# Performance work log

Measured on AMD Instinct MI355X. Metric: run time of the kernel, lower is better.

The kernel has to match this reference:

```python
import jax, jax.numpy as jnp
import numpy as np

B, T, D, E, K = 4, 2048, 2048, 8, 2
H = 4 * D  # expert hidden dim


def setup_inputs() -> dict:
    key = jax.random.key(0)
    ks = jax.random.split(key, 12)
    s = 0.02  # weight init scale
    return {
        "x": jax.random.normal(ks[0], (B, T, D), dtype=jnp.float32),
        "eps": jax.random.normal(ks[1], (B, T, E), dtype=jnp.float32),
        "Wr": jax.random.normal(ks[2], (D, E), dtype=jnp.float32) * s,
        "br": jnp.zeros((E,), dtype=jnp.float32),
        "Wn": jax.random.normal(ks[3], (D, E), dtype=jnp.float32) * s,
        "bn": jnp.zeros((E,), dtype=jnp.float32),
        "W1": jax.random.normal(ks[4], (E, D, H), dtype=jnp.float32) * s,
        "b1": jnp.zeros((E, H), dtype=jnp.float32),
        "W2": jax.random.normal(ks[5], (E, H, D), dtype=jnp.float32) * s,
        "b2": jnp.zeros((E, D), dtype=jnp.float32),
    }


def _moe(x, eps, Wr, br, Wn, bn, W1, b1, W2, b2):
    # --- noisy top-k router ---
    logits = x @ Wr + br                                   # [B,T,E]
    noise_logits = x @ Wn + bn                             # [B,T,E]
    noisy = logits + eps * jax.nn.softplus(noise_logits)   # [B,T,E]
    _, top_idx = jax.lax.top_k(noisy, K)                   # [B,T,K]
    sel = jax.nn.one_hot(top_idx, E, dtype=noisy.dtype).sum(-2)  # [B,T,E] 0/1
    neg_inf = jnp.asarray(-jnp.inf, dtype=noisy.dtype)
    sparse_logits = jnp.where(sel > 0, noisy, neg_inf)
    gates = jax.nn.softmax(sparse_logits, axis=-1)         # zeros off the top-k
    # --- expert MLPs, combined with gates (gate==0 exactly when unrouted,
    #     matching the torch masked gather/scatter; dropout in eval mode) ---
    out = jnp.zeros_like(x)
    for i in range(E):  # fixed small expert count
        h = jax.nn.relu(x @ W1[i] + b1[i])                 # [B,T,H]
        y = h @ W2[i] + b2[i]                              # [B,T,D]
        out = out + y * gates[..., i:i + 1]
    return out


def reference(x, eps, Wr, br, Wn, bn, W1, b1, W2, b2):
    return _moe(x, eps, Wr, br, Wn, bn, W1, b1, W2, b2)
```

## Files before the change

### kernel.cpp

```cpp
#include <hip/hip_runtime.h>

#define BT_TOK 8192
#define DDIM   2048
#define EEXP   8
#define HDIM   8192
#define MAXT1  72
#define MAXT2  144

typedef __bf16 bf16x8 __attribute__((ext_vector_type(8)));
typedef float  f32x4  __attribute__((ext_vector_type(4)));

__device__ inline ushort f2bf(float f) {
  unsigned u = __float_as_uint(f);
  u += 0x7FFFu + ((u >> 16) & 1u);
  return (ushort)(u >> 16);
}

__device__ __forceinline__ void gl16(const ushort* g, ushort* l) {
  __builtin_amdgcn_global_load_lds(
      (const __attribute__((address_space(1))) void*)g,
      (__attribute__((address_space(3))) void*)l, 16, 0, 0);
}

__global__ __launch_bounds__(256) void k_router(
    const float* __restrict__ x, const float* __restrict__ eps,
    const float* __restrict__ Wr, const float* __restrict__ br,
    const float* __restrict__ Wn, const float* __restrict__ bn,
    int* __restrict__ cnt, int* __restrict__ tk_e, int* __restrict__ tk_p,
    float* __restrict__ tk_g)
{
  const int lane = threadIdx.x & 63;
  const int t = blockIdx.x * 4 + (threadIdx.x >> 6);
  const float* xr = x + (size_t)t * DDIM;
  float aL[8] = {0,0,0,0,0,0,0,0};
  float aN[8] = {0,0,0,0,0,0,0,0};
  for (int i = lane; i < DDIM; i += 64) {
    float xv = xr[i];
    const float4* wr4 = (const float4*)(Wr + (size_t)i * EEXP);
    const float4* wn4 = (const float4*)(Wn + (size_t)i * EEXP);
    float4 r0 = wr4[0], r1 = wr4[1];
    float4 n0 = wn4[0], n1 = wn4[1];
    aL[0] += xv * r0.x; aL[1] += xv * r0.y; aL[2] += xv * r0.z; aL[3] += xv * r0.w;
    aL[4] += xv * r1.x; aL[5] += xv * r1.y; aL[6] += xv * r1.z; aL[7] += xv * r1.w;
    aN[0] += xv * n0.x; aN[1] += xv * n0.y; aN[2] += xv * n0.z; aN[3] += xv * n0.w;
    aN[4] += xv * n1.x; aN[5] += xv * n1.y; aN[6] += xv * n1.z; aN[7] += xv * n1.w;
  }
  #pragma unroll
  for (int e = 0; e < 8; ++e) {
    float v = aL[e];
    #pragma unroll
    for (int s = 32; s; s >>= 1) v += __shfl_xor(v, s);
    aL[e] = v;
    float w = aN[e];
    #pragma unroll
    for (int s = 32; s; s >>= 1) w += __shfl_xor(w, s);
    aN[e] = w;
  }
  float nz[8];
  #pragma unroll
  for (int e = 0; e < 8; ++e) {
    float l = aL[e] + br[e];
    float z = aN[e] + bn[e];
    float sp = fmaxf(z, 0.f) + log1pf(expf(-fabsf(z)));
    nz[e] = l + eps[(size_t)t * EEXP + e] * sp;
  }
  int e1 = 0; float v1 = nz[0];
  #pragma unroll
  for (int e = 1; e < 8; ++e) if (nz[e] > v1) { v1 = nz[e]; e1 = e; }
  int e2 = (e1 == 0) ? 1 : 0; float v2 = nz[e2];
  #pragma unroll
  for (int e = 0; e < 8; ++e) if (e != e1 && nz[e] > v2) { v2 = nz[e]; e2 = e; }
  float ex = expf(v2 - v1);
  float g1 = 1.f / (1.f + ex);
  float g2 = ex / (1.f + ex);
  if (lane == 0) {
    int p1 = atomicAdd(&cnt[e1], 1);
    int p2 = atomicAdd(&cnt[e2], 1);
    tk_e[t * 2 + 0] = e1; tk_p[t * 2 + 0] = p1; tk_g[t * 2 + 0] = g1;
    tk_e[t * 2 + 1] = e2; tk_p[t * 2 + 1] = p2; tk_g[t * 2 + 1] = g2;
  }
}

__global__ void k_off(const int* __restrict__ cnt, int* __restrict__ off,
                      int* __restrict__ tm1, int* __restrict__ tm2,
                      int* __restrict__ ntl) {
  if (threadIdx.x == 0 && blockIdx.x == 0) {
    int a = 0, n1 = 0, n2 = 0;
    for (int e = 0; e < EEXP; ++e) {
      off[e] = a;
      int mt = (cnt[e] + 255) >> 8;
      for (int m = 0; m < mt; ++m) {
        tm1[n1++] = (e << 8) | (m << 1);
        tm2[n2++] = (e << 8) | (m << 1);
        tm2[n2++] = (e << 8) | (m << 1) | 1;
      }
      a += cnt[e];
    }
    off[EEXP] = a;
    ntl[0] = n1; ntl[1] = n2;
  }
}

__global__ __launch_bounds__(256) void k_gather(
    const float* __restrict__ x, const int* __restrict__ off,
    const int* __restrict__ tk_e, const int* __restrict__ tk_p,
    const float* __restrict__ tk_g,
    int* __restrict__ slt, float* __restrict__ gate, ushort* __restrict__ xg)
{
  const int b = blockIdx.x;
  const int t = b >> 1;
  const int e = tk_e[b];
  const int slot = off[e] + tk_p[b];
  if (threadIdx.x == 0) { slt[b] = slot; gate[slot] = tk_g[b]; }
  const float4* src = (const float4*)(x + (size_t)t * DDIM);
  ushort* dst = xg + (size_t)slot * DDIM;
  const int i = threadIdx.x;
  float4 a = src[i * 2 + 0];
  float4 c = src[i * 2 + 1];
  union { ushort u[8]; uint4 q; } pk;
  pk.u[0] = f2bf(a.x); pk.u[1] = f2bf(a.y); pk.u[2] = f2bf(a.z); pk.u[3] = f2bf(a.w);
  pk.u[4] = f2bf(c.x); pk.u[5] = f2bf(c.y); pk.u[6] = f2bf(c.z); pk.u[7] = f2bf(c.w);
  *(uint4*)(dst + (size_t)i * 8) = pk.q;
}

__global__ __launch_bounds__(256) void k_transpose(
    const float* __restrict__ W, ushort* __restrict__ Wt, int R, int C)
{
  const int e = blockIdx.z;
  const float* We = W + (size_t)e * R * C;
  ushort* Wte = Wt + (size_t)e * R * C;
  const int r0 = blockIdx.y * 64, c0 = blockIdx.x * 64;
  __shared__ float tile[64][65];
  const int tx = threadIdx.x & 15, ty = threadIdx.x >> 4;
  #pragma unroll
  for (int p = 0; p < 4; ++p) {
    float4 v = *(const float4*)(We + (size_t)(r0 + p * 16 + ty) * C + c0 + tx * 4);
    tile[p * 16 + ty][tx * 4 + 0] = v.x;
    tile[p * 16 + ty][tx * 4 + 1] = v.y;
    tile[p * 16 + ty][tx * 4 + 2] = v.z;
    tile[p * 16 + ty][tx * 4 + 3] = v.w;
  }
  __syncthreads();
  const int c = threadIdx.x >> 2, rb = (threadIdx.x & 3) * 16;
  union { ushort u[16]; uint4 q[2]; } pk;
  #pragma unroll
  for (int j = 0; j < 16; ++j) pk.u[j] = f2bf(tile[rb + j][c]);
  uint4* dst = (uint4*)(Wte + (size_t)(c0 + c) * R + r0 + rb);
  dst[0] = pk.q[0];
  dst[1] = pk.q[1];
}


#define MFMA_(a, b, c) __builtin_amdgcn_mfma_f32_16x16x32_bf16(a, b, c, 0, 0, 0)
#define DSR(D, A) asm volatile("ds_read_b128 %0, %1" : "=v"(D) : "v"(A))
#define MQ(MB, NB, AV, BV) do {                                                  \
    _Pragma("unroll")                                                            \
    for (int i_ = 0; i_ < 4; ++i_) {                                             \
      acc[(MB)+i_][(NB)]   = MFMA_(AV[2*i_],   BV[0], acc[(MB)+i_][(NB)]);       \
      acc[(MB)+i_][(NB)+1] = MFMA_(AV[2*i_],   BV[2], acc[(MB)+i_][(NB)+1]);     \
    }                                                                            \
    _Pragma("unroll")                                                            \
    for (int i_ = 0; i_ < 4; ++i_) {                                             \
      acc[(MB)+i_][(NB)]   = MFMA_(AV[2*i_+1], BV[1], acc[(MB)+i_][(NB)]);       \
      acc[(MB)+i_][(NB)+1] = MFMA_(AV[2*i_+1], BV[3], acc[(MB)+i_][(NB)+1]);     \
    }                                                                            \
  } while (0)

template<int KD, int KSPLIT, int EPI, int NDIM>
__global__ __launch_bounds__(512, 2) void k_gemm(
    const ushort* __restrict__ A, const ushort* __restrict__ B,
    const float* __restrict__ bias, const int* __restrict__ off,
    const int* __restrict__ tileMap, const int* __restrict__ nT,
    const float* __restrict__ gate,
    ushort* __restrict__ Hout, float* __restrict__ Y)
{
  constexpr int KS = KD / KSPLIT;
  constexpr int NKT = KS / 64;
  constexpr int NTN = NDIM / 256;
  __shared__ ushort lds[65536];
  const int TM = nT[0];
  const int T = TM * NTN;

  const int bid = blockIdx.x;
  const int xcd = bid & 7, sl = bid >> 3;
  const int qq = T >> 3, rr = T & 7;
  const int base = xcd * qq + (xcd < rr ? xcd : rr);
  const int csz = qq + (xcd < rr ? 1 : 0);

  const int tid = threadIdx.x;
  const int lane = tid & 63, wid = tid >> 6;
  const int wm = wid >> 2, wn = wid & 3;
  const int fr = lane & 15, q2 = lane >> 4;
  const unsigned lbase =
      (unsigned)(size_t)(__attribute__((address_space(3))) ushort*)lds;
  const int swz = (q2 ^ (fr & 7)) * 16;
  const int aoff0 = (int)lbase + wm * 16384 + fr * 128 + swz;
  const int boff0 = (int)lbase + 32768 + wn * 8192 + fr * 128 + swz;
  const int trow = tid >> 3;
  const int kx = ((tid & 7) ^ (trow & 7)) * 8;
  const int dstA = tid * 8;

#define STG(SRC, DUS) gl16((SRC), &lds[DUS])

  for (int it = sl; it < csz; it += 32) {
    const int f = base + it;
    const int ni = (int)((unsigned)f / (unsigned)TM);
    const int pk = tileMap[f - ni * TM];
    const int e = pk >> 8, mi = (pk >> 1) & 127, kh = pk & 1;
    const int o = off[e], n_e = off[e + 1] - o;
    const int m0 = mi * 256;
    const int k0 = kh * KS;

    const ushort* Bex = B + (size_t)e * NDIM * KD + (size_t)ni * 256 * KD + k0 + kx;
    const ushort* aS[4]; const ushort* bS[4];
    #pragma unroll
    for (int j = 0; j < 4; ++j) {
      int ar = m0 + j * 64 + trow;
      if (ar > n_e - 1) ar = n_e - 1;
      aS[j] = A + (size_t)(o + ar) * KD + k0 + kx;
      bS[j] = Bex + (size_t)(j * 64 + trow) * KD;
    }

    f32x4 acc[8][4];
    #pragma unroll
    for (int m = 0; m < 8; ++m)
      #pragma unroll
      for (int n = 0; n < 4; ++n) acc[m][n] = (f32x4){0.f, 0.f, 0.f, 0.f};

    bf16x8 avL[8], avH[8], bvL[4], bvH[4];

    STG(aS[0], 0 + dstA);        STG(aS[2], 8192 + dstA);
    STG(aS[1], 4096 + dstA);     STG(aS[3], 12288 + dstA);
    STG(bS[0], 16384 + dstA);    STG(bS[1], 20480 + dstA);
    STG(bS[2], 24576 + dstA);    STG(bS[3], 28672 + dstA);
    STG(aS[0] + 64, 32768 + 0 + dstA);     STG(aS[2] + 64, 32768 + 8192 + dstA);
    STG(aS[1] + 64, 32768 + 4096 + dstA);  STG(aS[3] + 64, 32768 + 12288 + dstA);
    STG(bS[0] + 64, 32768 + 16384 + dstA); STG(bS[1] + 64, 32768 + 20480 + dstA);
    STG(bS[2] + 64, 32768 + 24576 + dstA); STG(bS[3] + 64, 32768 + 28672 + dstA);
    asm volatile("s_waitcnt vmcnt(8)");
    __builtin_amdgcn_s_barrier();
    __builtin_amdgcn_sched_barrier(0);
    {
      const int aA = aoff0, bA = boff0;
      DSR(avL[0], aA);        DSR(avL[1], aA ^ 64);
      DSR(avL[2], aA + 2048); DSR(avL[3], (aA + 2048) ^ 64);
      DSR(avL[4], aA + 4096); DSR(avL[5], (aA + 4096) ^ 64);
      DSR(avL[6], aA + 6144); DSR(avL[7], (aA + 6144) ^ 64);
      DSR(bvL[0], bA);        DSR(bvL[1], bA ^ 64);
      DSR(bvL[2], bA + 2048); DSR(bvL[3], (bA + 2048) ^ 64);
    }

    #pragma unroll 1
    for (int t = 0; t < NKT; ++t) {
      const int bb = (t & 1) << 16;
      const int aA = aoff0 + bb;
      const int bA = boff0 + bb;
      const int nbB = ((t + 1) & 1) << 16;
      const int aN = aoff0 + nbB;
      const int bN = boff0 + nbB;
      const int cbu = (t & 1) * 32768;
      const size_t ko = (size_t)(t + 2) * 64;
      const bool pf = (t + 2 < NKT);
      const bool rd1 = (t + 1 < NKT);

      DSR(avH[0], aA + 8192);         DSR(avH[1], (aA + 8192) ^ 64);
      DSR(avH[2], aA + 10240);        DSR(avH[3], (aA + 10240) ^ 64);
      DSR(avH[4], aA + 12288);        DSR(avH[5], (aA + 12288) ^ 64);
      DSR(avH[6], aA + 14336);        DSR(avH[7], (aA + 14336) ^ 64);
      __builtin_amdgcn_s_barrier();
      asm volatile("s_waitcnt lgkmcnt(8)");
      __builtin_amdgcn_sched_barrier(0);
      if (pf) { STG(aS[0] + ko, cbu + 0 + dstA); STG(aS[2] + ko, cbu + 8192 + dstA); }
      __builtin_amdgcn_s_setprio(1);
      MQ(0, 0, avL, bvL);
      __builtin_amdgcn_s_setprio(0);

      DSR(bvH[0], bA + 4096);  DSR(bvH[1], (bA + 4096) ^ 64);
      DSR(bvH[2], bA + 6144);  DSR(bvH[3], (bA + 6144) ^ 64);
      __builtin_amdgcn_s_barrier();
      asm volatile("s_waitcnt lgkmcnt(4)");
      __builtin_amdgcn_sched_barrier(0);
      if (pf) { STG(aS[1] + ko, cbu + 4096 + dstA); STG(aS[3] + ko, cbu + 12288 + dstA); }
      __builtin_amdgcn_s_setprio(1);
      MQ(4, 0, avH, bvL);
      __builtin_amdgcn_s_setprio(0);

      if (pf) asm volatile("s_waitcnt vmcnt(4)");
      else    asm volatile("s_waitcnt vmcnt(0)");
      __builtin_amdgcn_s_barrier();
      asm volatile("s_waitcnt lgkmcnt(0)");
      __builtin_amdgcn_sched_barrier(0);
      if (pf) {
        STG(bS[0] + ko, cbu + 16384 + dstA); STG(bS[1] + ko, cbu + 20480 + dstA);
        STG(bS[2] + ko, cbu + 24576 + dstA); STG(bS[3] + ko, cbu + 28672 + dstA);
      }
      __builtin_amdgcn_s_setprio(1);
      MQ(0, 2, avL, bvH);
      __builtin_amdgcn_s_setprio(0);
      if (rd1) {
        DSR(avL[0], aN);        DSR(avL[1], aN ^ 64);
        DSR(avL[2], aN + 2048); DSR(avL[3], (aN + 2048) ^ 64);
        DSR(avL[4], aN + 4096); DSR(avL[5], (aN + 4096) ^ 64);
        DSR(avL[6], aN + 6144); DSR(avL[7], (aN + 6144) ^ 64);
      }

      __builtin_amdgcn_s_barrier();
      __builtin_amdgcn_sched_barrier(0);
      if (rd1) {
        DSR(bvL[0], bN);        DSR(bvL[1], bN ^ 64);
        DSR(bvL[2], bN + 2048); DSR(bvL[3], (bN + 2048) ^ 64);
      }
      __builtin_amdgcn_s_setprio(1);
      MQ(4, 2, avH, bvH);
      __builtin_amdgcn_s_setprio(0);
    }

    asm volatile("s_waitcnt vmcnt(0)");
    const int colBase = ni * 256 + wn * 64 + fr;
    const int rBase = m0 + wm * 128 + q2 * 4;
    float bb4[4];
    #pragma unroll
    for (int n = 0; n < 4; ++n) {
      if constexpr (EPI == 0)
        bb4[n] = bias[(size_t)e * NDIM + colBase + n * 16];
      else
        bb4[n] = (kh == 0) ? bias[(size_t)e * NDIM + colBase + n * 16] : 0.f;
    }

    if constexpr (EPI == 0) {
      #pragma unroll
      for (int m = 0; m < 8; ++m) {
        #pragma unroll
        for (int jj = 0; jj < 4; ++jj) {
          int r = rBase + m * 16 + jj;
          if (r < n_e) {
            ushort* hp = Hout + (size_t)(o + r) * NDIM + colBase;
            #pragma unroll
            for (int n = 0; n < 4; ++n)
              hp[n * 16] = f2bf(fmaxf(acc[m][n][jj] + bb4[n], 0.f));
          }
        }
      }
    } else {
      float* yk = Y + ((size_t)kh << 25);
      #pragma unroll
      for (int m = 0; m < 8; ++m) {
        #pragma unroll
        for (int jj = 0; jj < 4; ++jj) {
          int r = rBase + m * 16 + jj;
          if (r < n_e) {
            float g = gate[o + r];
            float* yp = yk + (size_t)(o + r) * NDIM + colBase;
            #pragma unroll
            for (int n = 0; n < 4; ++n)
              yp[n * 16] = g * (acc[m][n][jj] + bb4[n]);
          }
        }
      }
    }
  }
#undef STG
}

__global__ __launch_bounds__(256) void k_combine(
    const float* __restrict__ Y, const int* __restrict__ slt,
    float* __restrict__ out)
{
  const int t = blockIdx.x;
  const int c = threadIdx.x * 8;
  const int sA = slt[t * 2], sB = slt[t * 2 + 1];
  const float4* pA0 = (const float4*)(Y + (size_t)sA * DDIM + c);
  const float4* pB0 = (const float4*)(Y + (size_t)sB * DDIM + c);
  const float4* pA1 = (const float4*)(Y + ((size_t)1 << 25) + (size_t)sA * DDIM + c);
  const float4* pB1 = (const float4*)(Y + ((size_t)1 << 25) + (size_t)sB * DDIM + c);
  float4* op = (float4*)(out + (size_t)t * DDIM + c);
  #pragma unroll
  for (int j = 0; j < 2; ++j) {
    float4 a = pA0[j], b = pA1[j], cc = pB0[j], d = pB1[j];
    float4 r;
    r.x = a.x + b.x + cc.x + d.x;
    r.y = a.y + b.y + cc.y + d.y;
    r.z = a.z + b.z + cc.z + d.z;
    r.w = a.w + b.w + cc.w + d.w;
    op[j] = r;
  }
}

extern "C" void kernel_launch(void* const* d_in, const int* in_sizes, int n_in,
                              void* d_out, int out_size, void* d_ws, size_t ws_size,
                              hipStream_t stream) {
  const float* x   = (const float*)d_in[0];
  const float* eps = (const float*)d_in[1];
  const float* Wr  = (const float*)d_in[2];
  const float* br  = (const float*)d_in[3];
  const float* Wn  = (const float*)d_in[4];
  const float* bn  = (const float*)d_in[5];
  const float* W1  = (const float*)d_in[6];
  const float* b1  = (const float*)d_in[7];
  const float* W2  = (const float*)d_in[8];
  const float* b2  = (const float*)d_in[9];
  float* out = (float*)d_out;

  char* p = (char*)d_ws;
  size_t used = 0;
  auto alloc = [&](size_t bytes) -> void* {
    void* r = p + used;
    used += (bytes + 255) & ~(size_t)255;
    return r;
  };
  int*    cnt   = (int*)alloc(EEXP * 4);
  int*    off   = (int*)alloc((EEXP + 1) * 4);
  int*    tm1   = (int*)alloc(MAXT1 * 4);
  int*    tm2   = (int*)alloc(MAXT2 * 4);
  int*    ntl   = (int*)alloc(2 * 4);
  int*    tk_e  = (int*)alloc(2 * BT_TOK * 4);
  int*    tk_p  = (int*)alloc(2 * BT_TOK * 4);
  float*  tk_g  = (float*)alloc(2 * BT_TOK * 4);
  int*    slt   = (int*)alloc(2 * BT_TOK * 4);
  float*  gate  = (float*)alloc(2 * BT_TOK * 4);
  ushort* xg    = (ushort*)alloc((size_t)2 * BT_TOK * DDIM * 2);
  ushort* Wt1   = (ushort*)alloc((size_t)EEXP * HDIM * DDIM * 2);
  ushort* Wt2   = (ushort*)alloc((size_t)EEXP * HDIM * DDIM * 2);
  ushort* hbuf  = (ushort*)alloc((size_t)2 * BT_TOK * HDIM * 2);
  if (used > ws_size) return;
  float* Yf = (float*)Wt1;

  hipMemsetAsync(cnt, 0, EEXP * 4, stream);

  k_router<<<BT_TOK / 4, 256, 0, stream>>>(x, eps, Wr, br, Wn, bn,
                                           cnt, tk_e, tk_p, tk_g);
  k_off<<<1, 64, 0, stream>>>(cnt, off, tm1, tm2, ntl);
  k_gather<<<2 * BT_TOK, 256, 0, stream>>>(x, off, tk_e, tk_p, tk_g, slt, gate, xg);

  {
    dim3 g1(HDIM / 64, DDIM / 64, EEXP);
    k_transpose<<<g1, 256, 0, stream>>>(W1, Wt1, DDIM, HDIM);
    dim3 g2(DDIM / 64, HDIM / 64, EEXP);
    k_transpose<<<g2, 256, 0, stream>>>(W2, Wt2, HDIM, DDIM);
  }

  k_gemm<DDIM, 1, 0, HDIM><<<256, 512, 0, stream>>>(xg, Wt1, b1, off, tm1, ntl,
                                                    gate, hbuf, Yf);
  k_gemm<HDIM, 2, 1, DDIM><<<256, 512, 0, stream>>>(hbuf, Wt2, b2, off, tm2, ntl + 1,
                                                    gate, hbuf, Yf);
  k_combine<<<BT_TOK, 256, 0, stream>>>(Yf, slt, out);
}
```

Baseline: 1.736 ms.

## Restructure GEMM main loop into two k-half fragment sets with merged prefetch

Reorganizes the LDS fragment reads and MFMA schedule from four quadrant phases per k-tile into two phases, each loading a full set of A/B fragments for one 32-wide k-half and issuing all 32 MFMAs. All global-to-LDS prefetches for the tile after next are now issued together after a single vmcnt(0) wait, and the number of barriers per iteration drops. This is meant to cut barrier and wait overhead and give longer MFMA runs, but it waits for all outstanding global loads mid-iteration, which may expose memory latency. It also adds an extra barrier before the initial staging.

```diff
diff --git a/kernel.cpp b/kernel.cpp
--- a/kernel.cpp
+++ b/kernel.cpp
@@ -153,17 +153,23 @@
 
 #define MFMA_(a, b, c) __builtin_amdgcn_mfma_f32_16x16x32_bf16(a, b, c, 0, 0, 0)
 #define DSR(D, A) asm volatile("ds_read_b128 %0, %1" : "=v"(D) : "v"(A))
-#define MQ(MB, NB, AV, BV) do {                                                  \
-    _Pragma("unroll")                                                            \
-    for (int i_ = 0; i_ < 4; ++i_) {                                             \
-      acc[(MB)+i_][(NB)]   = MFMA_(AV[2*i_],   BV[0], acc[(MB)+i_][(NB)]);       \
-      acc[(MB)+i_][(NB)+1] = MFMA_(AV[2*i_],   BV[2], acc[(MB)+i_][(NB)+1]);     \
-    }                                                                            \
-    _Pragma("unroll")                                                            \
-    for (int i_ = 0; i_ < 4; ++i_) {                                             \
-      acc[(MB)+i_][(NB)]   = MFMA_(AV[2*i_+1], BV[1], acc[(MB)+i_][(NB)]);       \
-      acc[(MB)+i_][(NB)+1] = MFMA_(AV[2*i_+1], BV[3], acc[(MB)+i_][(NB)+1]);     \
-    }                                                                            \
+
+#define DSET(FA, FB, AB, BB, XO) do {                                    \
+    DSR(FA[0], (AB) ^ (XO));          DSR(FA[1], ((AB)+2048) ^ (XO));    \
+    DSR(FA[2], ((AB)+4096) ^ (XO));   DSR(FA[3], ((AB)+6144) ^ (XO));    \
+    DSR(FA[4], ((AB)+8192) ^ (XO));   DSR(FA[5], ((AB)+10240) ^ (XO));   \
+    DSR(FA[6], ((AB)+12288) ^ (XO));  DSR(FA[7], ((AB)+14336) ^ (XO));   \
+    DSR(FB[0], (BB) ^ (XO));          DSR(FB[1], ((BB)+2048) ^ (XO));    \
+    DSR(FB[2], ((BB)+4096) ^ (XO));   DSR(FB[3], ((BB)+6144) ^ (XO));    \
+  } while (0)
+
+#define MSET(FA, FB) do {                                                \
+    _Pragma("unroll")                                                    \
+    for (int m_ = 0; m_ < 8; ++m_) {                                     \
+      _Pragma("unroll")                                                  \
+      for (int n_ = 0; n_ < 4; ++n_)                                     \
+        acc[m_][n_] = MFMA_(FA[m_], FB[n_], acc[m_][n_]);                \
+    }                                                                    \
   } while (0)
 
 template<int KD, int KSPLIT, int EPI, int NDIM>
@@ -227,28 +233,21 @@
       #pragma unroll
       for (int n = 0; n < 4; ++n) acc[m][n] = (f32x4){0.f, 0.f, 0.f, 0.f};
 
-    bf16x8 avL[8], avH[8], bvL[4], bvH[4];
-
-    STG(aS[0], 0 + dstA);        STG(aS[2], 8192 + dstA);
-    STG(aS[1], 4096 + dstA);     STG(aS[3], 12288 + dstA);
+    bf16x8 fa0[8], fb0[4], fa1[8], fb1[4];
+
+    __builtin_amdgcn_s_barrier();
+    STG(aS[0], 0 + dstA);        STG(aS[1], 4096 + dstA);
+    STG(aS[2], 8192 + dstA);     STG(aS[3], 12288 + dstA);
     STG(bS[0], 16384 + dstA);    STG(bS[1], 20480 + dstA);
     STG(bS[2], 24576 + dstA);    STG(bS[3], 28672 + dstA);
-    STG(aS[0] + 64, 32768 + 0 + dstA);     STG(aS[2] + 64, 32768 + 8192 + dstA);
-    STG(aS[1] + 64, 32768 + 4096 + dstA);  STG(aS[3] + 64, 32768 + 12288 + dstA);
+    STG(aS[0] + 64, 32768 + 0 + dstA);     STG(aS[1] + 64, 32768 + 4096 + dstA);
+    STG(aS[2] + 64, 32768 + 8192 + dstA);  STG(aS[3] + 64, 32768 + 12288 + dstA);
     STG(bS[0] + 64, 32768 + 16384 + dstA); STG(bS[1] + 64, 32768 + 20480 + dstA);
     STG(bS[2] + 64, 32768 + 24576 + dstA); STG(bS[3] + 64, 32768 + 28672 + dstA);
     asm volatile("s_waitcnt vmcnt(8)");
     __builtin_amdgcn_s_barrier();
     __builtin_amdgcn_sched_barrier(0);
-    {
-      const int aA = aoff0, bA = boff0;
-      DSR(avL[0], aA);        DSR(avL[1], aA ^ 64);
-      DSR(avL[2], aA + 2048); DSR(avL[3], (aA + 2048) ^ 64);
-      DSR(avL[4], aA + 4096); DSR(avL[5], (aA + 4096) ^ 64);
-      DSR(avL[6], aA + 6144); DSR(avL[7], (aA + 6144) ^ 64);
-      DSR(bvL[0], bA);        DSR(bvL[1], bA ^ 64);
-      DSR(bvL[2], bA + 2048); DSR(bvL[3], (bA + 2048) ^ 64);
-    }
+    DSET(fa0, fb0, aoff0, boff0, 0);
 
     #pragma unroll 1
     for (int t = 0; t < NKT; ++t) {
@@ -263,59 +262,32 @@
       const bool pf = (t + 2 < NKT);
       const bool rd1 = (t + 1 < NKT);
 
-      DSR(avH[0], aA + 8192);         DSR(avH[1], (aA + 8192) ^ 64);
-      DSR(avH[2], aA + 10240);        DSR(avH[3], (aA + 10240) ^ 64);
-      DSR(avH[4], aA + 12288);        DSR(avH[5], (aA + 12288) ^ 64);
-      DSR(avH[6], aA + 14336);        DSR(avH[7], (aA + 14336) ^ 64);
+      DSET(fa1, fb1, aA, bA, 64);
       __builtin_amdgcn_s_barrier();
-      asm volatile("s_waitcnt lgkmcnt(8)");
+      asm volatile("s_waitcnt lgkmcnt(12)");
       __builtin_amdgcn_sched_barrier(0);
-      if (pf) { STG(aS[0] + ko, cbu + 0 + dstA); STG(aS[2] + ko, cbu + 8192 + dstA); }
       __builtin_amdgcn_s_setprio(1);
-      MQ(0, 0, avL, bvL);
+      MSET(fa0, fb0);
       __builtin_amdgcn_s_setprio(0);
 
-      DSR(bvH[0], bA + 4096);  DSR(bvH[1], (bA + 4096) ^ 64);
-      DSR(bvH[2], bA + 6144);  DSR(bvH[3], (bA + 6144) ^ 64);
+      asm volatile("s_waitcnt vmcnt(0)");
       __builtin_amdgcn_s_barrier();
-      asm volatile("s_waitcnt lgkmcnt(4)");
-      __builtin_amdgcn_sched_barrier(0);
-      if (pf) { STG(aS[1] + ko, cbu + 4096 + dstA); STG(aS[3] + ko, cbu + 12288 + dstA); }
-      __builtin_amdgcn_s_setprio(1);
-      MQ(4, 0, avH, bvL);
-      __builtin_amdgcn_s_setprio(0);
-
-      if (pf) asm volatile("s_waitcnt vmcnt(4)");
-      else    asm volatile("s_waitcnt vmcnt(0)");
-      __builtin_amdgcn_s_barrier();
-      asm volatile("s_waitcnt lgkmcnt(0)");
+      if (rd1) DSET(fa0, fb0, aN, bN, 0);
+      if (rd1) asm volatile("s_waitcnt lgkmcnt(12)");
+      else     asm volatile("s_waitcnt lgkmcnt(0)");
       __builtin_amdgcn_sched_barrier(0);
       if (pf) {
+        STG(aS[0] + ko, cbu + 0 + dstA);     STG(aS[1] + ko, cbu + 4096 + dstA);
+        STG(aS[2] + ko, cbu + 8192 + dstA);  STG(aS[3] + ko, cbu + 12288 + dstA);
         STG(bS[0] + ko, cbu + 16384 + dstA); STG(bS[1] + ko, cbu + 20480 + dstA);
         STG(bS[2] + ko, cbu + 24576 + dstA); STG(bS[3] + ko, cbu + 28672 + dstA);
       }
       __builtin_amdgcn_s_setprio(1);
-      MQ(0, 2, avL, bvH);
-      __builtin_amdgcn_s_setprio(0);
-      if (rd1) {
-        DSR(avL[0], aN);        DSR(avL[1], aN ^ 64);
-        DSR(avL[2], aN + 2048); DSR(avL[3], (aN + 2048) ^ 64);
-        DSR(avL[4], aN + 4096); DSR(avL[5], (aN + 4096) ^ 64);
-        DSR(avL[6], aN + 6144); DSR(avL[7], (aN + 6144) ^ 64);
-      }
-
-      __builtin_amdgcn_s_barrier();
-      __builtin_amdgcn_sched_barrier(0);
-      if (rd1) {
-        DSR(bvL[0], bN);        DSR(bvL[1], bN ^ 64);
-        DSR(bvL[2], bN + 2048); DSR(bvL[3], (bN + 2048) ^ 64);
-      }
-      __builtin_amdgcn_s_setprio(1);
-      MQ(4, 2, avH, bvH);
+      MSET(fa1, fb1);
       __builtin_amdgcn_s_setprio(0);
     }
-
     asm volatile("s_waitcnt vmcnt(0)");
+
     const int colBase = ni * 256 + wn * 64 + fr;
     const int rBase = m0 + wm * 128 + q2 * 4;
     float bb4[4];
```

Result: slower. 1.803 ms (+3.9%).
